# Optimization experiments

Measured on AMD Instinct MI355X. Metric: run time of the kernel, lower is better.

Reference implementation:

```python
import jax, jax.numpy as jnp
import numpy as np

N = 8192
IN_DIM = 512
HID = 512


def setup_inputs() -> dict:
    key = jax.random.key(0)
    k1, k2, k3, k4 = jax.random.split(key, 4)
    input_features = jax.random.normal(k1, (N, IN_DIM), dtype=jnp.float32)
    # positive weighted adjacency so degrees > 0
    adjacency_matrix = jax.random.uniform(k2, (N, N), dtype=jnp.float32)
    # xavier_init: normal with std = 1/sqrt(in_dim/2)
    Wgcn1 = jax.random.normal(k3, (IN_DIM, HID), dtype=jnp.float32) * (1.0 / np.sqrt(IN_DIM / 2.0))
    bgcn1 = jnp.zeros((HID,), dtype=jnp.float32)
    Wgcn12 = jax.random.normal(k4, (HID, HID), dtype=jnp.float32) * (1.0 / np.sqrt(HID / 2.0))
    bgcn12 = jnp.zeros((HID,), dtype=jnp.float32)
    return {
        "input_features": input_features,
        "adjacency_matrix": adjacency_matrix,
        "Wgcn1": Wgcn1,
        "bgcn1": bgcn1,
        "Wgcn12": Wgcn12,
        "bgcn12": bgcn12,
    }


def reference(input_features, adjacency_matrix, Wgcn1, bgcn1, Wgcn12, bgcn12):
    # D^{-1/2} A D^{-1/2}: diag matmuls expressed as row/col elementwise scaling
    # (mathematically identical to torch.matmul(diag(d), A @ diag(d)))
    d_inv_sqrt = jnp.power(adjacency_matrix.sum(axis=1), -0.5)  # [N]
    norm_adj = d_inv_sqrt[:, None] * adjacency_matrix * d_inv_sqrt[None, :]  # [N, N]

    support = input_features @ Wgcn1            # [N, HID]
    out = norm_adj @ support + bgcn1            # [N, HID]
    out = jax.nn.relu(out)                      # dropout p=0.0 -> identity
    support = out @ Wgcn12                      # [N, HID]
    out = norm_adj @ support + bgcn12           # [N, HID]
    return out
```

## Files before the change

### kernel.cpp

```cpp
#include <hip/hip_runtime.h>
#include <stdint.h>


typedef __attribute__((ext_vector_type(8))) __bf16 bf16x8;
typedef __attribute__((ext_vector_type(4))) float f32x4;
typedef __attribute__((ext_vector_type(8))) unsigned short u16x8;

__device__ __forceinline__ unsigned short f2bf(float f) {
  union { float f; uint32_t u; } v; v.f = f;
  uint32_t u = v.u;
  return (unsigned short)((u + 0x7fffu + ((u >> 16) & 1u)) >> 16);
}

__device__ __forceinline__ float bf2f(unsigned short u) {
  union { uint32_t u; float f; } v; v.u = ((uint32_t)u) << 16; return v.f;
}

__device__ __forceinline__ void async_cp16(const void* g, void* lds) {
  auto gp = (const __attribute__((address_space(1))) uint32_t*)g;
  auto lp = (__attribute__((address_space(3))) uint32_t*)lds;
  __builtin_amdgcn_global_load_lds(gp, lp, 16, 0, 0);
}

__global__ __launch_bounds__(256) void k_rowsum_convert(
    const float* __restrict__ A, unsigned short* __restrict__ Abf,
    float* __restrict__ dvec, int ncols) {
  const int row = blockIdx.x;
  const float* arow = A + (size_t)row * ncols;
  unsigned short* orow = Abf + (size_t)row * ncols;
  float s = 0.f;
  for (int c = threadIdx.x * 4; c < ncols; c += 256 * 4) {
    float4 v = *(const float4*)(arow + c);
    s += (v.x + v.y) + (v.z + v.w);
    ushort4 o;
    o.x = f2bf(v.x); o.y = f2bf(v.y); o.z = f2bf(v.z); o.w = f2bf(v.w);
    *(ushort4*)(orow + c) = o;
  }
  #pragma unroll
  for (int off = 32; off > 0; off >>= 1) s += __shfl_down(s, off);
  __shared__ float red[4];
  if ((threadIdx.x & 63) == 0) red[threadIdx.x >> 6] = s;
  __syncthreads();
  if (threadIdx.x == 0) {
    float t = (red[0] + red[1]) + (red[2] + red[3]);
    dvec[row] = 1.0f / sqrtf(t);
  }
}

__global__ __launch_bounds__(256) void k_f32_to_bf16(
    const float* __restrict__ in, unsigned short* __restrict__ out, int n4) {
  int i = blockIdx.x * 256 + threadIdx.x;
  if (i < n4) {
    float4 v = ((const float4*)in)[i];
    ushort4 o;
    o.x = f2bf(v.x); o.y = f2bf(v.y); o.z = f2bf(v.z); o.w = f2bf(v.w);
    ((ushort4*)out)[i] = o;
  }
}

__global__ __launch_bounds__(256) void k_transpose_bf16(
    const float* __restrict__ in, unsigned short* __restrict__ out, int dim) {
  int o = blockIdx.x * 256 + threadIdx.x;
  if (o < dim * dim) {
    int k = o % dim;
    int n = o / dim;
    out[o] = f2bf(in[k * dim + n]);
  }
}

template <int MODE>
__global__ __launch_bounds__(256, 2) void gemm_bt(
    const unsigned short* __restrict__ Aop,
    const unsigned short* __restrict__ Bt,
    void* __restrict__ Cout,
    const float* __restrict__ dvec,
    const float* __restrict__ bias,
    int M, int N, int K) {
  constexpr int BM = 128, BN = 64, BK = 32;
  __shared__ unsigned short As[BM * BK];
  __shared__ unsigned short Bs[BN * BK];

  const int tid = threadIdx.x;
  const int w = tid >> 6;
  const int l = tid & 63;
  const int rowBase = blockIdx.y * BM;
  const int colBase = blockIdx.x * BN;
  const int waveM = w >> 1;
  const int waveN = w & 1;

  f32x4 acc[4][2];
  const f32x4 fz = {0.f, 0.f, 0.f, 0.f};
  #pragma unroll
  for (int m = 0; m < 4; ++m)
    #pragma unroll
    for (int n = 0; n < 2; ++n) acc[m][n] = fz;

  const int chunkRow = l >> 2;
  const int kOff = (l & 3) * 8;
  const unsigned short* gA0 = Aop + (size_t)(rowBase + w * 16 + chunkRow) * K + kOff;
  const unsigned short* gA1 = gA0 + (size_t)64 * K;
  const unsigned short* gB0 = Bt + (size_t)(colBase + w * 16 + chunkRow) * K + kOff;
  unsigned short* lA0 = As + w * 512;
  unsigned short* lA1 = As + (w + 4) * 512;
  unsigned short* lB0 = Bs + w * 512;

  const int kfrag = (l >> 4) * 8;
  const int lrow = l & 15;

  for (int k0 = 0; k0 < K; k0 += BK) {
    async_cp16(gA0 + k0, lA0);
    async_cp16(gA1 + k0, lA1);
    async_cp16(gB0 + k0, lB0);
    __syncthreads();

    bf16x8 af[4], bfr[2];
    #pragma unroll
    for (int m = 0; m < 4; ++m)
      af[m] = *(const bf16x8*)(As + (waveM * 64 + m * 16 + lrow) * BK + kfrag);
    #pragma unroll
    for (int n = 0; n < 2; ++n)
      bfr[n] = *(const bf16x8*)(Bs + (waveN * 32 + n * 16 + lrow) * BK + kfrag);

    #pragma unroll
    for (int m = 0; m < 4; ++m)
      #pragma unroll
      for (int n = 0; n < 2; ++n)
        acc[m][n] = __builtin_amdgcn_mfma_f32_16x16x32_bf16(af[m], bfr[n],
                                                            acc[m][n], 0, 0, 0);
    __syncthreads();
  }

  const int erow0 = rowBase + waveM * 64 + (l >> 4) * 4;
  const int ecol0 = colBase + waveN * 32 + (l & 15);
  #pragma unroll
  for (int m = 0; m < 4; ++m) {
    #pragma unroll
    for (int n = 0; n < 2; ++n) {
      #pragma unroll
      for (int j = 0; j < 4; ++j) {
        const int rowg = erow0 + m * 16 + j;
        const int colg = ecol0 + n * 16;
        float v = acc[m][n][j];
        if (MODE == 0) {
          v *= dvec[colg];
          ((unsigned short*)Cout)[(size_t)rowg * N + colg] = f2bf(v);
        }
      }
    }
  }
}

__global__ __launch_bounds__(512, 1) void gemm_big8(
    const unsigned short* __restrict__ Aop,
    const unsigned short* __restrict__ Bt,
    unsigned short* __restrict__ Pout,
    int M, int N, int K, int kLen) {
  constexpr int BK = 64;
  __shared__ char lds[131072];

  const int tid = threadIdx.x;
  const int w = tid >> 6;
  const int l = tid & 63;
  const int rowBase = blockIdx.y * 256;
  const int colBase = blockIdx.x * 256;
  const int kBase = blockIdx.z * kLen;
  const int waveM = w >> 2;
  const int waveN = w & 3;

  f32x4 acc[8][4];
  const f32x4 fz = {0.f, 0.f, 0.f, 0.f};
  #pragma unroll
  for (int m = 0; m < 8; ++m)
    #pragma unroll
    for (int n = 0; n < 4; ++n) acc[m][n] = fz;

  const int swzElem = ((l & 7) ^ ((l >> 3) & 7)) * 8;
  const unsigned short* aSrc =
      Aop + (size_t)(rowBase + w * 16 + (l >> 3)) * K + kBase + swzElem;
  const unsigned short* bSrc =
      Bt + (size_t)(colBase + w * 16 + (l >> 3)) * K + kBase + swzElem;
  const int dstTh = w * 2048 + l * 16;

#define STAGE_TILE(tt, bufbase)                                               \
  {                                                                           \
    const size_t tOff = (size_t)(tt) * BK;                                    \
    async_cp16(aSrc + tOff,                    lds + (bufbase) + dstTh);      \
    async_cp16(bSrc + tOff,                    lds + (bufbase) + 32768 + dstTh); \
    async_cp16(aSrc + (size_t)8 * K + tOff,    lds + (bufbase) + 1024 + dstTh);  \
    async_cp16(bSrc + (size_t)8 * K + tOff,    lds + (bufbase) + 32768 + 1024 + dstTh); \
    async_cp16(aSrc + (size_t)128 * K + tOff,  lds + (bufbase) + 16384 + dstTh); \
    async_cp16(bSrc + (size_t)128 * K + tOff,  lds + (bufbase) + 32768 + 16384 + dstTh); \
    async_cp16(aSrc + (size_t)136 * K + tOff,  lds + (bufbase) + 16384 + 1024 + dstTh); \
    async_cp16(bSrc + (size_t)136 * K + tOff,  lds + (bufbase) + 32768 + 16384 + 1024 + dstTh); \
  }

  const int nt = kLen / BK;
  STAGE_TILE(0, 0);
  STAGE_TILE(1, 65536);

  const int lrow = l & 15;
  const int kq = l >> 4;
  const int xr = l & 7;
  const int aRowByte = (waveM * 128 + lrow) * 128;
  const int bRowByte = (waveN * 64 + lrow) * 128;

  for (int t = 0; t < nt; ++t) {
    const int curbase = (t & 1) * 65536;
    if (t == nt - 1) {
      asm volatile("s_waitcnt vmcnt(0)\n\ts_barrier" ::: "memory");
    } else {
      asm volatile("s_waitcnt vmcnt(8)\n\ts_barrier" ::: "memory");
    }

    bf16x8 bfr[4];
    #pragma unroll
    for (int ph = 0; ph < 4; ++ph) {
      const int kk = ph >> 1, mh = ph & 1;
      const int kbyteS = ((kk * 4 + kq) ^ xr) << 4;
      bf16x8 af[4];
      #pragma unroll
      for (int i = 0; i < 4; ++i)
        af[i] = *(const bf16x8*)(lds + curbase + aRowByte +
                                 (mh * 64 + i * 16) * 128 + kbyteS);
      if (mh == 0) {
        #pragma unroll
        for (int n = 0; n < 4; ++n)
          bfr[n] = *(const bf16x8*)(lds + curbase + 32768 + bRowByte +
                                    n * 16 * 128 + kbyteS);
      }
      __builtin_amdgcn_s_barrier();
      __builtin_amdgcn_s_setprio(1);
      #pragma unroll
      for (int i = 0; i < 4; ++i)
        #pragma unroll
        for (int n = 0; n < 4; ++n)
          acc[mh * 4 + i][n] = __builtin_amdgcn_mfma_f32_16x16x32_bf16(
              af[i], bfr[n], acc[mh * 4 + i][n], 0, 0, 0);
      __builtin_amdgcn_s_setprio(0);
    }
    asm volatile("s_barrier" ::: "memory");
    if (t + 2 < nt) STAGE_TILE(t + 2, curbase);
  }
#undef STAGE_TILE

  unsigned short* pz = Pout + (size_t)blockIdx.z * M * N;
  const int erow0 = rowBase + waveM * 128 + (l >> 4) * 4;
  const int ecol0 = colBase + waveN * 64 + (l & 15);
  #pragma unroll
  for (int m = 0; m < 8; ++m) {
    #pragma unroll
    for (int n = 0; n < 4; ++n) {
      #pragma unroll
      for (int j = 0; j < 4; ++j) {
        pz[(size_t)(erow0 + m * 16 + j) * N + ecol0 + n * 16] =
            f2bf(acc[m][n][j]);
      }
    }
  }
}

template <int MODE>
__global__ __launch_bounds__(256) void k_reduce(
    const unsigned short* __restrict__ parts,
    const float* __restrict__ dvec,
    const float* __restrict__ bias,
    void* __restrict__ outp, int M, int N) {
  const size_t MN = (size_t)M * N;
  const size_t idx = ((size_t)blockIdx.x * 256 + threadIdx.x) * 8;
  if (idx >= MN) return;
  const int row = (int)(idx / N);
  const int col = (int)(idx % N);
  const float di = dvec[row];
  float s[8] = {0, 0, 0, 0, 0, 0, 0, 0};
  #pragma unroll
  for (int z = 0; z < 4; ++z) {
    u16x8 v = *(const u16x8*)(parts + z * MN + idx);
    #pragma unroll
    for (int e = 0; e < 8; ++e) s[e] += bf2f(v[e]);
  }
  if (MODE == 1) {
    ushort4 o0, o1;
    unsigned short tmp[8];
    #pragma unroll
    for (int e = 0; e < 8; ++e) {
      float v = di * s[e] + bias[col + e];
      v = v > 0.f ? v : 0.f;
      tmp[e] = f2bf(v);
    }
    o0.x = tmp[0]; o0.y = tmp[1]; o0.z = tmp[2]; o0.w = tmp[3];
    o1.x = tmp[4]; o1.y = tmp[5]; o1.z = tmp[6]; o1.w = tmp[7];
    *(ushort4*)((unsigned short*)outp + idx) = o0;
    *(ushort4*)((unsigned short*)outp + idx + 4) = o1;
  } else {
    float4 o0, o1;
    o0.x = di * s[0] + bias[col + 0];
    o0.y = di * s[1] + bias[col + 1];
    o0.z = di * s[2] + bias[col + 2];
    o0.w = di * s[3] + bias[col + 3];
    o1.x = di * s[4] + bias[col + 4];
    o1.y = di * s[5] + bias[col + 5];
    o1.z = di * s[6] + bias[col + 6];
    o1.w = di * s[7] + bias[col + 7];
    *(float4*)((float*)outp + idx) = o0;
    *(float4*)((float*)outp + idx + 4) = o1;
  }
}

extern "C" void kernel_launch(void* const* d_in, const int* in_sizes, int n_in,
                              void* d_out, int out_size, void* d_ws, size_t ws_size,
                              hipStream_t stream) {
  const float* X  = (const float*)d_in[0];
  const float* A  = (const float*)d_in[1];
  const float* W1 = (const float*)d_in[2];
  const float* b1 = (const float*)d_in[3];
  const float* W2 = (const float*)d_in[4];
  const float* b2 = (const float*)d_in[5];
  float* out = (float*)d_out;

  constexpr int NN = 8192, IN = 512, HID = 512;
  constexpr int KSPLIT = 4;

  char* ws = (char*)d_ws;
  float* ddeg = (float*)ws;
  unsigned short* Abf = (unsigned short*)(ws + (32 << 10));
  unsigned short* W1t = Abf + (size_t)NN * NN;
  unsigned short* W2t = W1t + IN * HID;
  unsigned short* P0  = W2t + HID * HID;
  unsigned short* P1  = P0 + (size_t)NN * HID;
  unsigned short* parts = P1 + (size_t)NN * HID;

  k_rowsum_convert<<<NN, 256, 0, stream>>>(A, Abf, ddeg, NN);
  k_f32_to_bf16<<<(NN * IN / 4 + 255) / 256, 256, 0, stream>>>(X, P0, NN * IN / 4);
  k_transpose_bf16<<<(IN * HID + 255) / 256, 256, 0, stream>>>(W1, W1t, IN);
  k_transpose_bf16<<<(HID * HID + 255) / 256, 256, 0, stream>>>(W2, W2t, HID);

  gemm_bt<0><<<dim3(NN / 64, HID / 128), 256, 0, stream>>>(
      W1t, P0, P1, ddeg, nullptr, HID, NN, IN);
  gemm_big8<<<dim3(HID / 256, NN / 256, KSPLIT), 512, 0, stream>>>(
      Abf, P1, parts, NN, HID, NN, NN / KSPLIT);
  k_reduce<1><<<(int)((size_t)NN * HID / 8 / 256), 256, 0, stream>>>(
      parts, ddeg, b1, P0, NN, HID);
  gemm_bt<0><<<dim3(NN / 64, HID / 128), 256, 0, stream>>>(
      W2t, P0, P1, ddeg, nullptr, HID, NN, HID);
  gemm_big8<<<dim3(HID / 256, NN / 256, KSPLIT), 512, 0, stream>>>(
      Abf, P1, parts, NN, HID, NN, NN / KSPLIT);
  k_reduce<2><<<(int)((size_t)NN * HID / 8 / 256), 256, 0, stream>>>(
      parts, ddeg, b2, out, NN, HID);
}
```

Measured before the change: 279.6 us.

## Switch big GEMM to triple-buffered BK=32 pipeline with split A/B staging

Replaces the double-buffered BK=64 adjacency GEMM with a three-buffer ring of BK=32 tiles. The A and B loads for the tile two steps ahead are issued between the two MFMA halves, and the swizzle is adapted to 64-byte rows. The goal is to overlap global-to-LDS copies with compute more finely and shorten barrier stalls. In exchange it doubles the number of loop iterations and barriers per K, and the three-buffer WAR ordering depends on the barrier placement.

```diff
diff --git a/kernel.cpp b/kernel.cpp
--- a/kernel.cpp
+++ b/kernel.cpp
@@ -150,13 +150,13 @@
   }
 }
 
-__global__ __launch_bounds__(512, 1) void gemm_big8(
+__global__ __launch_bounds__(512, 1) void gemm_big3(
     const unsigned short* __restrict__ Aop,
     const unsigned short* __restrict__ Bt,
     unsigned short* __restrict__ Pout,
     int M, int N, int K, int kLen) {
-  constexpr int BK = 64;
-  __shared__ char lds[131072];
+  constexpr int BK = 32;
+  __shared__ char lds[3 * 32768];
 
   const int tid = threadIdx.x;
   const int w = tid >> 6;
@@ -174,74 +174,83 @@
     #pragma unroll
     for (int n = 0; n < 4; ++n) acc[m][n] = fz;
 
-  const int swzElem = ((l & 7) ^ ((l >> 3) & 7)) * 8;
+  const int srcElem = ((l & 3) ^ ((l >> 3) & 3)) * 8;
   const unsigned short* aSrc =
-      Aop + (size_t)(rowBase + w * 16 + (l >> 3)) * K + kBase + swzElem;
+      Aop + (size_t)(rowBase + w * 32 + (l >> 2)) * K + kBase + srcElem;
   const unsigned short* bSrc =
-      Bt + (size_t)(colBase + w * 16 + (l >> 3)) * K + kBase + swzElem;
+      Bt + (size_t)(colBase + w * 32 + (l >> 2)) * K + kBase + srcElem;
   const int dstTh = w * 2048 + l * 16;
 
-#define STAGE_TILE(tt, bufbase)                                               \
-  {                                                                           \
-    const size_t tOff = (size_t)(tt) * BK;                                    \
-    async_cp16(aSrc + tOff,                    lds + (bufbase) + dstTh);      \
-    async_cp16(bSrc + tOff,                    lds + (bufbase) + 32768 + dstTh); \
-    async_cp16(aSrc + (size_t)8 * K + tOff,    lds + (bufbase) + 1024 + dstTh);  \
-    async_cp16(bSrc + (size_t)8 * K + tOff,    lds + (bufbase) + 32768 + 1024 + dstTh); \
-    async_cp16(aSrc + (size_t)128 * K + tOff,  lds + (bufbase) + 16384 + dstTh); \
-    async_cp16(bSrc + (size_t)128 * K + tOff,  lds + (bufbase) + 32768 + 16384 + dstTh); \
-    async_cp16(aSrc + (size_t)136 * K + tOff,  lds + (bufbase) + 16384 + 1024 + dstTh); \
-    async_cp16(bSrc + (size_t)136 * K + tOff,  lds + (bufbase) + 32768 + 16384 + 1024 + dstTh); \
+#define STAGE_A(tt, bb)                                                   \
+  {                                                                       \
+    const size_t o = (size_t)(tt) * BK;                                   \
+    async_cp16(aSrc + o, lds + (bb) + dstTh);                             \
+    async_cp16(aSrc + (size_t)16 * K + o, lds + (bb) + dstTh + 1024);     \
+  }
+#define STAGE_B(tt, bb)                                                   \
+  {                                                                       \
+    const size_t o = (size_t)(tt) * BK;                                   \
+    async_cp16(bSrc + o, lds + (bb) + 16384 + dstTh);                     \
+    async_cp16(bSrc + (size_t)16 * K + o, lds + (bb) + 16384 + dstTh + 1024); \
   }
 
   const int nt = kLen / BK;
-  STAGE_TILE(0, 0);
-  STAGE_TILE(1, 65536);
+  STAGE_A(0, 0); STAGE_B(0, 0);
+  STAGE_A(1, 32768); STAGE_B(1, 32768);
 
   const int lrow = l & 15;
   const int kq = l >> 4;
-  const int xr = l & 7;
-  const int aRowByte = (waveM * 128 + lrow) * 128;
-  const int bRowByte = (waveN * 64 + lrow) * 128;
-
+  const int xr = (lrow >> 1) & 3;
+  const int slotByte = ((kq ^ xr) << 4);
+  const int aRow0 = (waveM * 128 + lrow) * 64;
+  const int bRow0 = 16384 + (waveN * 64 + lrow) * 64;
+
+  int cur = 0, nxt = 32768, fut = 65536;
   for (int t = 0; t < nt; ++t) {
-    const int curbase = (t & 1) * 65536;
     if (t == nt - 1) {
-      asm volatile("s_waitcnt vmcnt(0)\n\ts_barrier" ::: "memory");
+      asm volatile("s_waitcnt vmcnt(0)" ::: "memory");
     } else {
-      asm volatile("s_waitcnt vmcnt(8)\n\ts_barrier" ::: "memory");
+      asm volatile("s_waitcnt vmcnt(4)" ::: "memory");
     }
-
-    bf16x8 bfr[4];
-    #pragma unroll
-    for (int ph = 0; ph < 4; ++ph) {
-      const int kk = ph >> 1, mh = ph & 1;
-      const int kbyteS = ((kk * 4 + kq) ^ xr) << 4;
-      bf16x8 af[4];
-      #pragma unroll
-      for (int i = 0; i < 4; ++i)
-        af[i] = *(const bf16x8*)(lds + curbase + aRowByte +
-                                 (mh * 64 + i * 16) * 128 + kbyteS);
-      if (mh == 0) {
-        #pragma unroll
-        for (int n = 0; n < 4; ++n)
-          bfr[n] = *(const bf16x8*)(lds + curbase + 32768 + bRowByte +
-                                    n * 16 * 128 + kbyteS);
-      }
-      __builtin_amdgcn_s_barrier();
-      __builtin_amdgcn_s_setprio(1);
-      #pragma unroll
-      for (int i = 0; i < 4; ++i)
-        #pragma unroll
-        for (int n = 0; n < 4; ++n)
-          acc[mh * 4 + i][n] = __builtin_amdgcn_mfma_f32_16x16x32_bf16(
-              af[i], bfr[n], acc[mh * 4 + i][n], 0, 0, 0);
-      __builtin_amdgcn_s_setprio(0);
-    }
-    asm volatile("s_barrier" ::: "memory");
-    if (t + 2 < nt) STAGE_TILE(t + 2, curbase);
-  }
-#undef STAGE_TILE
+    __builtin_amdgcn_s_barrier();
+
+    bf16x8 af[4], bfr[4];
+    #pragma unroll
+    for (int i = 0; i < 4; ++i)
+      af[i] = *(const bf16x8*)(lds + cur + aRow0 + i * 16 * 64 + slotByte);
+    #pragma unroll
+    for (int n = 0; n < 4; ++n)
+      bfr[n] = *(const bf16x8*)(lds + cur + bRow0 + n * 16 * 64 + slotByte);
+    if (t + 2 < nt) STAGE_A(t + 2, fut);
+    __builtin_amdgcn_s_barrier();
+    __builtin_amdgcn_s_setprio(1);
+    #pragma unroll
+    for (int i = 0; i < 4; ++i)
+      #pragma unroll
+      for (int n = 0; n < 4; ++n)
+        acc[i][n] = __builtin_amdgcn_mfma_f32_16x16x32_bf16(
+            af[i], bfr[n], acc[i][n], 0, 0, 0);
+    __builtin_amdgcn_s_setprio(0);
+
+    bf16x8 af2[4];
+    #pragma unroll
+    for (int i = 0; i < 4; ++i)
+      af2[i] = *(const bf16x8*)(lds + cur + aRow0 + (64 + i * 16) * 64 + slotByte);
+    if (t + 2 < nt) STAGE_B(t + 2, fut);
+    __builtin_amdgcn_s_barrier();
+    __builtin_amdgcn_s_setprio(1);
+    #pragma unroll
+    for (int i = 0; i < 4; ++i)
+      #pragma unroll
+      for (int n = 0; n < 4; ++n)
+        acc[4 + i][n] = __builtin_amdgcn_mfma_f32_16x16x32_bf16(
+            af2[i], bfr[n], acc[4 + i][n], 0, 0, 0);
+    __builtin_amdgcn_s_setprio(0);
+
+    const int tmp = cur; cur = nxt; nxt = fut; fut = tmp;
+  }
+#undef STAGE_A
+#undef STAGE_B
 
   unsigned short* pz = Pout + (size_t)blockIdx.z * M * N;
   const int erow0 = rowBase + waveM * 128 + (l >> 4) * 4;
@@ -336,13 +345,13 @@
 
   gemm_bt<0><<<dim3(NN / 64, HID / 128), 256, 0, stream>>>(
       W1t, P0, P1, ddeg, nullptr, HID, NN, IN);
-  gemm_big8<<<dim3(HID / 256, NN / 256, KSPLIT), 512, 0, stream>>>(
+  gemm_big3<<<dim3(HID / 256, NN / 256, KSPLIT), 512, 0, stream>>>(
       Abf, P1, parts, NN, HID, NN, NN / KSPLIT);
   k_reduce<1><<<(int)((size_t)NN * HID / 8 / 256), 256, 0, stream>>>(
       parts, ddeg, b1, P0, NN, HID);
   gemm_bt<0><<<dim3(NN / 64, HID / 128), 256, 0, stream>>>(
       W2t, P0, P1, ddeg, nullptr, HID, NN, HID);
-  gemm_big8<<<dim3(HID / 256, NN / 256, KSPLIT), 512, 0, stream>>>(
+  gemm_big3<<<dim3(HID / 256, NN / 256, KSPLIT), 512, 0, stream>>>(
       Abf, P1, parts, NN, HID, NN, NN / KSPLIT);
   k_reduce<2><<<(int)((size_t)NN * HID / 8 / 256), 256, 0, stream>>>(
       parts, ddeg, b2, out, NN, HID);
```

New measurement: 267.0 us. -4.5%, faster.
